# Kernel tuning notes

Measured on AMD Instinct MI355X. Metric: run time of the kernel, lower is better.

Reference implementation:

```python
import math
import jax, jax.numpy as jnp
import numpy as np

B, S, HIDDEN = 1, 8192, 2048
NUM_HEADS = 16
HEAD_DIM = HIDDEN // NUM_HEADS
NUM_FW = 4
FW_DIM = HIDDEN // NUM_FW
D_H = FW_DIM  # inter_multi = 1.0
WINDOW = 256
CHUNK = 2048
ROPE_THETA = 500000.0
BASE_LR_INV = float(np.log(np.expm1(0.001)))  # inv_softplus(1e-3)


def rms_norm(x, w, eps=1e-6):
    return x * jax.lax.rsqrt(jnp.mean(x * x, axis=-1, keepdims=True) + eps) * w


def apply_rope(q, k, theta):
    D = q.shape[-1]
    inv = 1.0 / (theta ** (jnp.arange(0, D, 2, dtype=jnp.float32) / D))
    t = jnp.arange(q.shape[1], dtype=jnp.float32)
    f = t[:, None] * inv[None, :]  # [S, D/2]
    cos = jnp.cos(f)[None, :, None, :]
    sin = jnp.sin(f)[None, :, None, :]
    def ap(x):
        x1, x2 = jnp.split(x, 2, axis=-1)
        return jnp.concatenate([x1 * cos - x2 * sin, x2 * cos + x1 * sin], axis=-1)
    return ap(q), ap(k)


def sliding_window_attn(q, k, v, window):
    # q,k,v: [B,S,H,D]; causal window of `window` tokens incl. self (flash (window-1, 0))
    B_, S_, H_, D_ = q.shape
    W = window
    nc = S_ // W
    def blk(x):
        return x.transpose(0, 2, 1, 3).reshape(B_, H_, nc, W, D_)
    qb, kb, vb = blk(q), blk(k), blk(v)
    pad = jnp.zeros((B_, H_, 1, W, D_), q.dtype)
    k2 = jnp.concatenate([jnp.concatenate([pad, kb[:, :, :-1]], 2), kb], 3)  # [B,H,nc,2W,D]
    v2 = jnp.concatenate([jnp.concatenate([pad, vb[:, :, :-1]], 2), vb], 3)
    r = jnp.arange(W)[:, None]
    j = jnp.arange(2 * W)[None, :]
    base = (j >= r + 1) & (j <= W + r)  # causal + within-window
    keypos = (jnp.arange(nc)[:, None, None] - 1) * W + j[None]
    mask = base[None] & (keypos >= 0)  # [nc,W,2W]
    scores = jnp.einsum('bhnqd,bhnkd->bhnqk', qb, k2) * (1.0 / math.sqrt(D_))
    scores = jnp.where(mask[None, None], scores, -jnp.inf)
    p = jax.nn.softmax(scores, axis=-1)
    o = jnp.einsum('bhnqk,bhnkd->bhnqd', p, v2)
    return o.reshape(B_, H_, S_, D_).transpose(0, 2, 1, 3)


def ttt_swiglu(fq, fk, fv, l0, l1, l2, w0, w1, w2, chunk):
    # fq/fk/fv: [BN,S,d]; l*: [BN,S,1]; w0,w2: [BN,dh,d]; w1: [BN,d,dh]
    BN, S_, d = fq.shape
    nc = S_ // chunk
    def ch(x):
        return x.reshape(BN, nc, chunk, x.shape[-1]).transpose(1, 0, 2, 3)
    xs = (ch(fq), ch(fk), ch(fv), ch(l0), ch(l1), ch(l2))
    def step(carry, x):
        w0c, w1c, w2c = carry
        qi, ki, vi, lr0, lr1, lr2 = x
        # apply current fast weights to chunk queries (SwiGLU MLP)
        o = jnp.einsum('bch,boh->bco',
                       jax.nn.silu(jnp.einsum('bcd,bhd->bch', qi, w0c)) * jnp.einsum('bcd,bhd->bch', qi, w2c),
                       w1c)
        # manual gradient of dot-product TTT loss L = -sum(v * f(k))
        g = jnp.einsum('bcd,bhd->bch', ki, w0c)
        hm = jnp.einsum('bcd,bhd->bch', ki, w2c)
        sg = jax.nn.sigmoid(g)
        silu_g = g * sg
        hid = silu_g * hm
        dhid = jnp.einsum('bco,boh->bch', vi, w1c)
        dhm = dhid * silu_g
        dg = dhid * hm
        dgp = dg * (sg * (1.0 + g * (1.0 - sg)))  # silu backprop
        w0n = w0c + jnp.einsum('bch,bcd->bhd', dgp * lr0, ki)
        w2n = w2c + jnp.einsum('bch,bcd->bhd', dhm * lr2, ki)
        w1n = w1c + jnp.einsum('bco,bch->boh', vi * lr1, hid)
        return (w0n, w1n, w2n), o
    _, outs = jax.lax.scan(step, (w0, w1, w2), xs)
    return outs.transpose(1, 0, 2, 3).reshape(BN, S_, d)


def setup_inputs():
    key = jax.random.key(0)
    ks = jax.random.split(key, 8)
    h = HIDDEN
    return {
        'hidden_states': jax.random.normal(ks[0], (B, S, h), jnp.float32),
        'qkv_w': jax.random.normal(ks[1], (3 * h, h), jnp.float32) * 0.02,
        'q_norm_w': jnp.ones((h,), jnp.float32),
        'k_norm_w': jnp.ones((h,), jnp.float32),
        'qk_scale': jnp.ones((h, 2), jnp.float32),
        'qk_offset': jnp.zeros((h, 2), jnp.float32),
        'lr_w': jax.random.normal(ks[2], (3 * NUM_FW, h), jnp.float32) * 0.02,
        'lr_b': jnp.zeros((3 * NUM_FW,), jnp.float32),
        'w0': jax.random.normal(ks[3], (NUM_FW, D_H, FW_DIM), jnp.float32) / math.sqrt(FW_DIM),
        'w1': jax.random.normal(ks[4], (NUM_FW, FW_DIM, D_H), jnp.float32) / math.sqrt(D_H),
        'w2': jax.random.normal(ks[5], (NUM_FW, D_H, FW_DIM), jnp.float32) / math.sqrt(FW_DIM),
        'ttt_norm_w': jnp.ones((FW_DIM,), jnp.float32),
        'o_proj_w': jax.random.normal(ks[6], (h, h), jnp.float32) * 0.02,
    }


def reference(hidden_states, qkv_w, q_norm_w, k_norm_w, qk_scale, qk_offset,
              lr_w, lr_b, w0, w1, w2, ttt_norm_w, o_proj_w):
    qkv = hidden_states @ qkv_w.T
    q, k, v = jnp.split(qkv, 3, axis=-1)
    q = rms_norm(q, q_norm_w)
    k = rms_norm(k, k_norm_w)
    # rescale q/k for the fast-weight path
    fq = q * qk_scale[:, 0] + qk_offset[:, 0]
    fk = k * qk_scale[:, 1] + qk_offset[:, 1]
    fv = v
    # windowed RoPE attention path
    qh = q.reshape(B, S, NUM_HEADS, HEAD_DIM)
    kh = k.reshape(B, S, NUM_HEADS, HEAD_DIM)
    vh = v.reshape(B, S, NUM_HEADS, HEAD_DIM)
    qh, kh = apply_rope(qh, kh, ROPE_THETA)
    attn_o = sliding_window_attn(qh, kh, vh, WINDOW).reshape(B, S, HIDDEN)
    # fast-weight (TTT) path: silu + per-head l2-norm on q/k
    fq = jax.nn.silu(fq).reshape(B, S, NUM_FW, FW_DIM)
    fk = jax.nn.silu(fk).reshape(B, S, NUM_FW, FW_DIM)
    fv = jax.nn.silu(fv).reshape(B, S, NUM_FW, FW_DIM)
    fq = fq / jnp.maximum(jnp.linalg.norm(fq, axis=-1, keepdims=True), 1e-12)
    fk = fk / jnp.maximum(jnp.linalg.norm(fk, axis=-1, keepdims=True), 1e-12)
    def flat(x):
        return x.transpose(0, 2, 1, 3).reshape(B * NUM_FW, S, FW_DIM)
    # per-token learning rates (mamba parameterization)
    lr = jax.nn.softplus(hidden_states @ lr_w.T + lr_b + BASE_LR_INV)  # [B,S,3*NH]
    l0, l1, l2 = jnp.split(lr, 3, axis=-1)
    def flat_lr(x):
        return x.transpose(0, 2, 1).reshape(B * NUM_FW, S, 1)
    def bcast(w):
        return jnp.broadcast_to(w[None], (B,) + w.shape).reshape(B * NUM_FW, w.shape[1], w.shape[2])
    o_fast = ttt_swiglu(flat(fq), flat(fk), flat(fv),
                        flat_lr(l0), flat_lr(l1), flat_lr(l2),
                        bcast(w0), bcast(w1), bcast(w2), CHUNK)
    o_fast = rms_norm(o_fast.reshape(B, NUM_FW, S, FW_DIM), ttt_norm_w)
    o_fast = o_fast.transpose(0, 2, 1, 3).reshape(B, S, HIDDEN)
    return (attn_o + o_fast) @ o_proj_w.T
```

## Files before the change

kernel.cpp:

```cpp
#include <hip/hip_runtime.h>
#include <hip/hip_bf16.h>

typedef __hip_bfloat16 bf16;
typedef __bf16 bft;
typedef bft bf16x8 __attribute__((ext_vector_type(8)));
typedef bft bf16x4 __attribute__((ext_vector_type(4)));
typedef float f32x4 __attribute__((ext_vector_type(4)));

#define S_LEN 8192
#define HID   2048
#define QKV3  6144
#define NH    16
#define HD    128
#define NFW   4
#define FD    512
#define CHUNK_LEN 2048
#define NCHUNK 4
#define BASE_LR_INV (-6.9072552f)
#define QKP 136
#define VSP 72
#define PSP 76

__device__ __forceinline__ float bf2f(bf16 x){ return __bfloat162float(x); }
__device__ __forceinline__ bf16  f2bf(float x){ return __float2bfloat16(x); }
__device__ __forceinline__ float sigm(float x){ return 1.f/(1.f+__expf(-x)); }
__device__ __forceinline__ float siluf(float x){ return x/(1.f+__expf(-x)); }
__device__ __forceinline__ float wave_sum(float v){
  #pragma unroll
  for(int off=32; off; off>>=1) v += __shfl_xor(v, off, 64);
  return v;
}

template<int N>
__device__ __forceinline__ void waitcnt_vm(){
  static_assert(N==0||N==2||N==4||N==8, "unsupported vmcnt");
  if constexpr (N==0)      asm volatile("s_waitcnt vmcnt(0)" ::: "memory");
  else if constexpr (N==2) asm volatile("s_waitcnt vmcnt(2)" ::: "memory");
  else if constexpr (N==4) asm volatile("s_waitcnt vmcnt(4)" ::: "memory");
  else                     asm volatile("s_waitcnt vmcnt(8)" ::: "memory");
}

__device__ __forceinline__ void bar(){
  __builtin_amdgcn_s_barrier();
  asm volatile("" ::: "memory");
}

template<int ROWS>
__device__ __forceinline__ void stage(const bft* __restrict__ src, long ld,
                                      bft* dst, int tid)
{
  const int lane = tid & 63, wv = tid >> 6;
  #pragma unroll
  for (int i = 0; i < ROWS/64; ++i) {
    const int r0 = wv*16 + i*64;
    const int row = r0 + (lane >> 2);
    const int g = (lane & 3) ^ ((row >> 1) & 3);
    const bft* gp = src + (size_t)row*ld + g*8;
    bft* lp = dst + (size_t)r0*32;
    __builtin_amdgcn_global_load_lds(
        (const __attribute__((address_space(1))) void*)gp,
        (__attribute__((address_space(3))) void*)lp, 16, 0, 0);
  }
}

template<int BM,int BN,int EPI>
__global__ __launch_bounds__(256) void mgemm_k(
    const bft* __restrict__ A, const bft* __restrict__ B, void* __restrict__ Cv,
    bft* __restrict__ Cd, bft* __restrict__ Ct, int K,
    long lda, long ldb, long ldc, long sA, long sB, long sC, long sCd)
{
  constexpr int AM = BM/32, AN = BN/32;
  constexpr int LPT = BM/64 + BN/64;
  __shared__ __align__(16) bft As[4][BM*32];
  __shared__ __align__(16) bft Bs[4][BN*32];
  const int tid = threadIdx.x;
  const int z = blockIdx.z;
  A += (size_t)z * sA;
  B += (size_t)z * sB;
  const size_t m0 = (size_t)blockIdx.y * BM, n0 = (size_t)blockIdx.x * BN;
  const int wv = tid >> 6, lane = tid & 63;
  const int wm = (wv & 1) * (BM/2), wn = (wv >> 1) * (BN/2);
  const int fr = lane & 15;
  const int fsw = ((lane >> 4) ^ ((fr >> 1) & 3)) * 8;

  f32x4 acc[AM][AN];
  #pragma unroll
  for (int i=0;i<AM;i++)
    #pragma unroll
    for (int j=0;j<AN;j++) acc[i][j] = (f32x4){0.f,0.f,0.f,0.f};

  const bft* Ab = A + m0*lda;
  const bft* Bb = B + n0*ldb;
  const int NS = K >> 5;

  stage<BM>(Ab,      lda, As[0], tid);
  stage<BN>(Bb,      ldb, Bs[0], tid);
  stage<BM>(Ab + 32, lda, As[1], tid);
  stage<BN>(Bb + 32, ldb, Bs[1], tid);
  waitcnt_vm<LPT>();
  bar();

  bf16x8 aP[AM], bP[AN], aQ[AM], bQ[AN];
  #pragma unroll
  for (int mi=0; mi<AM; mi++)
    aP[mi] = *(const bf16x8*)(As[0] + (size_t)(wm + mi*16 + fr)*32 + fsw);
  #pragma unroll
  for (int ni=0; ni<AN; ni++)
    bP[ni] = *(const bf16x8*)(Bs[0] + (size_t)(wn + ni*16 + fr)*32 + fsw);

  auto body = [&](bf16x8 (&ac)[AM], bf16x8 (&bc)[AN],
                  bf16x8 (&an)[AM], bf16x8 (&bn)[AN], int s){
    const int kt = (s + 2) * 32;
    const bool st2 = (s + 2 < NS);
    const bool rd  = (s + 1 < NS);
    if (st2) {
      stage<BM>(Ab + kt, lda, As[(s+2)&3], tid);
      stage<BN>(Bb + kt, ldb, Bs[(s+2)&3], tid);
    }
    if (rd) {
      if (st2) waitcnt_vm<LPT>(); else waitcnt_vm<0>();
      bar();
      const bft* An = As[(s+1)&3];
      const bft* Bn = Bs[(s+1)&3];
      #pragma unroll
      for (int mi=0; mi<AM; mi++)
        an[mi] = *(const bf16x8*)(An + (size_t)(wm + mi*16 + fr)*32 + fsw);
      #pragma unroll
      for (int ni=0; ni<AN; ni++)
        bn[ni] = *(const bf16x8*)(Bn + (size_t)(wn + ni*16 + fr)*32 + fsw);
    }
    __builtin_amdgcn_s_setprio(1);
    #pragma unroll
    for (int mi=0; mi<AM; mi++)
      #pragma unroll
      for (int ni=0; ni<AN; ni++)
        acc[mi][ni] = __builtin_amdgcn_mfma_f32_16x16x32_bf16(ac[mi], bc[ni], acc[mi][ni], 0, 0, 0);
    __builtin_amdgcn_s_setprio(0);
  };

  for (int s = 0; s < NS; s += 2) {
    body(aP, bP, aQ, bQ, s);
    body(aQ, bQ, aP, bP, s + 1);
  }

  const int er = (lane >> 4) * 4;
  const int ec = lane & 15;
  #pragma unroll
  for (int mi=0; mi<AM; mi++){
    #pragma unroll
    for (int ni=0; ni<AN; ni++){
      #pragma unroll
      for (int r=0; r<4; r++){
        size_t row = m0 + wm + mi*16 + er + r;
        size_t col = n0 + wn + ni*16 + ec;
        size_t idx = (size_t)z*sC + row*ldc + col;
        float v = acc[mi][ni][r];
        if constexpr (EPI == 0){
          ((bft*)Cv)[idx] = (bft)v;
        } else if constexpr (EPI == 1){
          ((float*)Cv)[idx] = v;
        } else {
          float nv = ((float*)Cv)[idx] + v;
          ((float*)Cv)[idx] = nv;
          Cd[(size_t)z*sCd + row*ldc + col] = (bft)nv;
          if (Ct) Ct[(size_t)z*FD*FD + col*FD + row] = (bft)nv;
        }
      }
    }
  }
}

template<int BM,int BN,int EPI>
static inline void mgemm(hipStream_t st, const bft* A, const bft* B, void* C,
    bft* Cd, bft* Ct, int M, int N, int K, long lda, long ldb, long ldc,
    int batch, long sA, long sB, long sC, long sCd)
{
  dim3 g(N/BN, M/BM, batch);
  mgemm_k<BM,BN,EPI><<<g, 256, 0, st>>>(A, B, C, Cd, Ct, K, lda, ldb, ldc, sA, sB, sC, sCd);
}

__device__ __forceinline__ void stage8(const bft* __restrict__ src, long ld,
                                       bft* dst, int tid)
{
  const int lane = tid & 63, wv = tid >> 6;
  #pragma unroll
  for (int i = 0; i < 2; ++i) {
    const int r0 = wv*16 + i*128;
    const int row = r0 + (lane >> 2);
    const int g = (lane & 3) ^ ((row >> 1) & 3);
    const bft* gp = src + (size_t)row*ld + g*8;
    bft* lp = dst + (size_t)r0*32;
    __builtin_amdgcn_global_load_lds(
        (const __attribute__((address_space(1))) void*)gp,
        (__attribute__((address_space(3))) void*)lp, 16, 0, 0);
  }
}

template<int EPI>
__global__ __launch_bounds__(512, 2) void mgemm8_k(
    const bft* __restrict__ A, const bft* __restrict__ B, void* __restrict__ Cv,
    int K, long lda, long ldb, long ldc)
{
  __shared__ __align__(16) bft As[4][256*32];
  __shared__ __align__(16) bft Bs[4][256*32];
  const int tid = threadIdx.x;

  const int gx = (int)gridDim.x;
  const int nwg = (int)(gridDim.x * gridDim.y);
  int lin = (int)(blockIdx.y * gridDim.x + blockIdx.x);
  if ((nwg & 7) == 0) lin = (lin & 7) * (nwg >> 3) + (lin >> 3);
  const size_t m0 = (size_t)(lin / gx) * 256;
  const size_t n0 = (size_t)(lin % gx) * 256;

  const int wv = tid >> 6, lane = tid & 63;
  const int wm = (wv & 1) * 128, wn = (wv >> 1) * 64;
  const int fr = lane & 15;
  const int fsw = ((lane >> 4) ^ ((fr >> 1) & 3)) * 8;

  f32x4 acc[8][4];
  #pragma unroll
  for (int i=0;i<8;i++)
    #pragma unroll
    for (int j=0;j<4;j++) acc[i][j] = (f32x4){0.f,0.f,0.f,0.f};

  const bft* Ab = A + m0*lda;
  const bft* Bb = B + n0*ldb;
  const int NS = K >> 5;

  stage8(Ab,      lda, As[0], tid);
  stage8(Bb,      ldb, Bs[0], tid);
  stage8(Ab + 32, lda, As[1], tid);
  stage8(Bb + 32, ldb, Bs[1], tid);
  waitcnt_vm<4>();
  bar();

  bf16x8 aP[8], bP[4], aQ[8], bQ[4];
  #pragma unroll
  for (int mi=0; mi<8; mi++)
    aP[mi] = *(const bf16x8*)(As[0] + (size_t)(wm + mi*16 + fr)*32 + fsw);
  #pragma unroll
  for (int ni=0; ni<4; ni++)
    bP[ni] = *(const bf16x8*)(Bs[0] + (size_t)(wn + ni*16 + fr)*32 + fsw);

  auto body = [&](bf16x8 (&ac)[8], bf16x8 (&bc)[4],
                  bf16x8 (&an)[8], bf16x8 (&bn)[4], int s){
    const int kt = (s + 2) * 32;
    const bool st2 = (s + 2 < NS);
    const bool rd  = (s + 1 < NS);
    if (st2) {
      stage8(Ab + kt, lda, As[(s+2)&3], tid);
      stage8(Bb + kt, ldb, Bs[(s+2)&3], tid);
    }
    if (rd) {
      if (st2) waitcnt_vm<4>(); else waitcnt_vm<0>();
      bar();
      const bft* An = As[(s+1)&3];
      const bft* Bn = Bs[(s+1)&3];
      #pragma unroll
      for (int mi=0; mi<8; mi++)
        an[mi] = *(const bf16x8*)(An + (size_t)(wm + mi*16 + fr)*32 + fsw);
      #pragma unroll
      for (int ni=0; ni<4; ni++)
        bn[ni] = *(const bf16x8*)(Bn + (size_t)(wn + ni*16 + fr)*32 + fsw);
    }
    __builtin_amdgcn_s_setprio(1);
    #pragma unroll
    for (int mi=0; mi<8; mi++)
      #pragma unroll
      for (int ni=0; ni<4; ni++)
        acc[mi][ni] = __builtin_amdgcn_mfma_f32_16x16x32_bf16(ac[mi], bc[ni], acc[mi][ni], 0, 0, 0);
    __builtin_amdgcn_s_setprio(0);
  };

  for (int s = 0; s < NS; s += 2) {
    body(aP, bP, aQ, bQ, s);
    body(aQ, bQ, aP, bP, s + 1);
  }

  const int er = (lane >> 4) * 4;
  const int ec = lane & 15;
  #pragma unroll
  for (int mi=0; mi<8; mi++){
    #pragma unroll
    for (int ni=0; ni<4; ni++){
      #pragma unroll
      for (int r=0; r<4; r++){
        size_t row = m0 + wm + mi*16 + er + r;
        size_t col = n0 + wn + ni*16 + ec;
        size_t idx = row*ldc + col;
        float v = acc[mi][ni][r];
        if constexpr (EPI == 0) ((bft*)Cv)[idx] = (bft)v;
        else                    ((float*)Cv)[idx] = v;
      }
    }
  }
}

template<int EPI>
static inline void mgemm8(hipStream_t st, const bft* A, const bft* B, void* C,
                          int M, int N, int K, long lda, long ldb, long ldc)
{
  dim3 g(N/256, M/256, 1);
  mgemm8_k<EPI><<<g, 512, 0, st>>>(A, B, C, K, lda, ldb, ldc);
}

__global__ __launch_bounds__(256) void cvt_k(const float* __restrict__ s,
    bft* __restrict__ d)
{
  size_t i = ((size_t)blockIdx.x*256 + threadIdx.x) * 8;
  const float4 v0 = *(const float4*)(s + i);
  const float4 v1 = *(const float4*)(s + i + 4);
  bf16x8 b;
  b[0]=(bft)v0.x; b[1]=(bft)v0.y; b[2]=(bft)v0.z; b[3]=(bft)v0.w;
  b[4]=(bft)v1.x; b[5]=(bft)v1.y; b[6]=(bft)v1.z; b[7]=(bft)v1.w;
  *(bf16x8*)(d + i) = b;
}

__global__ __launch_bounds__(256) void tr_k(const bft* __restrict__ in,
    bft* __restrict__ out, long ldin, long sIn, long sOut)
{
  __shared__ __align__(16) bft t[64][72];
  const int c0 = blockIdx.x*64, r0 = blockIdx.y*64;
  in  += (size_t)blockIdx.z * sIn;
  out += (size_t)blockIdx.z * sOut;
  const int tid = threadIdx.x;
  #pragma unroll
  for (int i=0;i<2;i++){
    int e = tid + i*256;
    int r = e >> 3, c8 = (e & 7) * 8;
    *(bf16x8*)&t[r][c8] = *(const bf16x8*)(in + (size_t)(r0+r)*ldin + c0 + c8);
  }
  __syncthreads();
  #pragma unroll
  for (int i=0;i<2;i++){
    int e = tid + i*256;
    int c = e >> 3, r8 = (e & 7) * 8;
    bf16x8 v;
    #pragma unroll
    for (int j=0;j<8;j++) v[j] = t[r8+j][c];
    *(bf16x8*)(out + (size_t)(c0+c)*CHUNK_LEN + r0 + r8) = v;
  }
}

__global__ __launch_bounds__(256) void tcw1_k(const float* __restrict__ w1,
    bft* __restrict__ w1tb)
{
  size_t idx = (size_t)blockIdx.x*256 + threadIdx.x;
  int z = (int)(idx >> 18);
  int h = (int)((idx >> 9) & 511);
  int o = (int)(idx & 511);
  w1tb[idx] = (bft)w1[(size_t)z*FD*FD + (size_t)o*FD + h];
}

__global__ __launch_bounds__(256) void vt_k(const bf16* __restrict__ qkv,
    bft* __restrict__ vT)
{
  __shared__ __align__(16) bft t[64*QKP];
  const int s0 = blockIdx.x * 64;
  const int h  = blockIdx.y;
  const int tid = threadIdx.x;
  #pragma unroll
  for (int i=0;i<4;i++){
    int e = tid + i*256;
    int rr = e >> 4, doff = (e & 15) * 8;
    *(bf16x8*)(t + rr*QKP + doff) =
        *(const bf16x8*)((const bft*)qkv + (size_t)(s0+rr)*QKV3 + 2*HID + h*HD + doff);
  }
  __syncthreads();
  #pragma unroll
  for (int it=0; it<4; it++){
    int d = (tid >> 3) + it*32;
    int so8 = (tid & 7) * 8;
    bf16x8 v;
    #pragma unroll
    for (int j=0;j<8;j++) v[j] = t[(so8+j)*QKP + d];
    *(bf16x8*)(vT + ((size_t)(h*HD + d))*S_LEN + s0 + so8) = v;
  }
}

__global__ void rope_k(float* __restrict__ rc, float* __restrict__ rs){
  int pos = blockIdx.x, d = threadIdx.x;
  float inv = 1.f / powf(500000.0f, (float)d * (1.0f/64.0f));
  float ang = (float)pos * inv;
  rc[pos*64+d] = cosf(ang);
  rs[pos*64+d] = sinf(ang);
}

__global__ __launch_bounds__(256) void lr_k(const float* __restrict__ hidden,
    const float* __restrict__ lr_w, const float* __restrict__ lr_b,
    float* __restrict__ lro)
{
  __shared__ float hrow[HID];
  __shared__ float red[4][12];
  int s = blockIdx.x, tid = threadIdx.x;
  for(int i=0;i<HID/256;i++) hrow[tid+256*i] = hidden[(size_t)s*HID + tid + 256*i];
  __syncthreads();
  float part[12];
  #pragma unroll
  for(int o=0;o<12;o++) part[o]=0.f;
  for(int i=0;i<HID/256;i++){
    int j = tid + 256*i;
    float h = hrow[j];
    #pragma unroll
    for(int o=0;o<12;o++) part[o] += h * lr_w[o*HID + j];
  }
  int lane = tid & 63, w = tid >> 6;
  #pragma unroll
  for(int o=0;o<12;o++){
    float v = wave_sum(part[o]);
    if(lane==0) red[w][o] = v;
  }
  __syncthreads();
  if(tid < 12){
    float v = red[0][tid]+red[1][tid]+red[2][tid]+red[3][tid] + lr_b[tid] + BASE_LR_INV;
    float sp = (v > 20.f) ? v : log1pf(expf(v));
    lro[s*12 + tid] = sp;
  }
}

__global__ __launch_bounds__(256) void e2a_k(
    bf16* __restrict__ qkv,
    const float* __restrict__ qnw, const float* __restrict__ knw)
{
  __shared__ float red[8];
  int s = blockIdx.x, tid = threadIdx.x;
  int lane = tid & 63, w = tid >> 6;
  float qv[8], kv[8];
  float sq = 0.f, sk = 0.f;
  size_t base = (size_t)s*QKV3;
  #pragma unroll
  for(int i=0;i<8;i++){
    int j = tid*8 + i;
    qv[i] = bf2f(qkv[base + j]);
    kv[i] = bf2f(qkv[base + HID + j]);
    sq += qv[i]*qv[i]; sk += kv[i]*kv[i];
  }
  sq = wave_sum(sq); sk = wave_sum(sk);
  if(lane==0){ red[w] = sq; red[4+w] = sk; }
  __syncthreads();
  float rq = rsqrtf((red[0]+red[1]+red[2]+red[3])*(1.f/HID) + 1e-6f);
  float rk = rsqrtf((red[4]+red[5]+red[6]+red[7])*(1.f/HID) + 1e-6f);
  #pragma unroll
  for(int i=0;i<8;i++){
    int j = tid*8 + i;
    qkv[base + j]       = f2bf(qv[i]*rq*qnw[j]);
    qkv[base + HID + j] = f2bf(kv[i]*rk*knw[j]);
  }
}

__global__ __launch_bounds__(256) void e2b_k(
    bf16* __restrict__ qkv,
    const float* __restrict__ qks, const float* __restrict__ qko)
{
  int s = blockIdx.x, tid = threadIdx.x;
  size_t base = (size_t)s*QKV3;
  float a[8], b[8], vv[8];
  float ga = 0.f, gb2 = 0.f;
  #pragma unroll
  for(int i=0;i<8;i++){
    int j = tid*8 + i;
    float qn = bf2f(qkv[base + j]);
    float kn = bf2f(qkv[base + HID + j]);
    float v  = bf2f(qkv[base + 2*HID + j]);
    a[i] = siluf(qn*qks[2*j]   + qko[2*j]);
    b[i] = siluf(kn*qks[2*j+1] + qko[2*j+1]);
    vv[i] = siluf(v);
    ga += a[i]*a[i]; gb2 += b[i]*b[i];
  }
  ga = wave_sum(ga); gb2 = wave_sum(gb2);
  float iq = 1.f / fmaxf(sqrtf(ga), 1e-12f);
  float ik = 1.f / fmaxf(sqrtf(gb2), 1e-12f);
  #pragma unroll
  for(int i=0;i<8;i++){
    int j = tid*8 + i;
    qkv[base + j]         = f2bf(a[i]*iq);
    qkv[base + HID + j]   = f2bf(b[i]*ik);
    qkv[base + 2*HID + j] = f2bf(vv[i]);
  }
}

__global__ __launch_bounds__(256) void attn_k(
    const bf16* __restrict__ qkv, const bft* __restrict__ vT,
    const float* __restrict__ rc, const float* __restrict__ rs,
    float* __restrict__ attn)
{
  __shared__ __align__(16) bft Qs[64*QKP];
  __shared__ __align__(16) bft Ks[64*QKP];
  __shared__ __align__(16) bft Vs[128*VSP];
  __shared__ __align__(16) bft Ps[64*PSP];
  const int head = blockIdx.x >> 7;
  const int Q0 = (blockIdx.x & 127) * 64;
  const int tid = threadIdx.x;
  const int hb = head * HD;
  const int lane = tid & 63;
  const int wm = (tid >> 6) * 16;
  const int fr = lane & 15, fko = (lane >> 4) * 8;
  const int rbase = (lane >> 4) * 4;

  #pragma unroll
  for(int i=0;i<16;i++){
    int e = tid + i*256;
    int rr = e >> 6, d = e & 63;
    int qpos = Q0 + rr;
    size_t b = (size_t)qpos*QKV3 + hb;
    float x1 = bf2f(qkv[b + d]);
    float x2 = bf2f(qkv[b + d + 64]);
    float c = rc[qpos*64 + d], sn = rs[qpos*64 + d];
    Qs[rr*QKP + d]      = (bft)(x1*c - x2*sn);
    Qs[rr*QKP + d + 64] = (bft)(x2*c + x1*sn);
  }
  __syncthreads();
  bf16x8 qf[4];
  #pragma unroll
  for (int kk=0;kk<4;kk++)
    qf[kk] = *(const bf16x8*)(Qs + (wm+fr)*QKP + kk*32 + fko);

  f32x4 Ot[8];
  #pragma unroll
  for (int i=0;i<8;i++) Ot[i] = (f32x4){0.f,0.f,0.f,0.f};
  float m4[4], l4[4];
  #pragma unroll
  for (int r=0;r<4;r++){ m4[r] = -INFINITY; l4[r] = 0.f; }

  for (int kt=0; kt<5; kt++){
    const int kb = Q0 - 256 + kt*64;
    if (kb < 0) continue;
    __syncthreads();
    #pragma unroll
    for(int i=0;i<16;i++){
      int e = tid + i*256;
      int rr = e >> 6, d = e & 63;
      int kpos = kb + rr;
      size_t b = (size_t)kpos*QKV3 + HID + hb;
      float x1 = bf2f(qkv[b + d]);
      float x2 = bf2f(qkv[b + d + 64]);
      float c = rc[kpos*64 + d], sn = rs[kpos*64 + d];
      Ks[rr*QKP + d]      = (bft)(x1*c - x2*sn);
      Ks[rr*QKP + d + 64] = (bft)(x2*c + x1*sn);
    }
    {
      int d = tid >> 1, koff = (tid & 1) * 32;
      const bft* vrow = vT + ((size_t)(hb + d))*S_LEN + kb + koff;
      bft* lrow = Vs + d*VSP + koff;
      #pragma unroll
      for (int j8=0;j8<4;j8++)
        *(bf16x8*)(lrow + j8*8) = *(const bf16x8*)(vrow + j8*8);
    }
    __syncthreads();

    f32x4 st[4];
    #pragma unroll
    for (int nt=0;nt<4;nt++){
      f32x4 acc = (f32x4){0.f,0.f,0.f,0.f};
      #pragma unroll
      for (int kk=0;kk<4;kk++){
        bf16x8 kf = *(const bf16x8*)(Ks + (nt*16+fr)*QKP + kk*32 + fko);
        acc = __builtin_amdgcn_mfma_f32_16x16x32_bf16(qf[kk], kf, acc, 0, 0, 0);
      }
      st[nt] = acc;
    }

    float pv[4][4];
    #pragma unroll
    for (int r=0;r<4;r++){
      int qpos = Q0 + wm + rbase + r;
      float sm[4];
      float mx = -INFINITY;
      #pragma unroll
      for (int nt=0;nt<4;nt++){
        int kpos = kb + nt*16 + fr;
        bool valid = (kpos > qpos - 256) && (kpos <= qpos);
        float s = valid ? st[nt][r] * 0.088388347648318447f : -INFINITY;
        sm[nt] = s;
        mx = fmaxf(mx, s);
      }
      mx = fmaxf(mx, __shfl_xor(mx, 1, 64));
      mx = fmaxf(mx, __shfl_xor(mx, 2, 64));
      mx = fmaxf(mx, __shfl_xor(mx, 4, 64));
      mx = fmaxf(mx, __shfl_xor(mx, 8, 64));
      float mnew = fmaxf(m4[r], mx);
      float alpha = (mnew == -INFINITY) ? 1.f : __expf(m4[r] - mnew);
      float ps = 0.f;
      #pragma unroll
      for (int nt=0;nt<4;nt++){
        float p = (sm[nt] == -INFINITY) ? 0.f : __expf(sm[nt] - mnew);
        pv[nt][r] = p;
        ps += p;
      }
      ps += __shfl_xor(ps, 1, 64);
      ps += __shfl_xor(ps, 2, 64);
      ps += __shfl_xor(ps, 4, 64);
      ps += __shfl_xor(ps, 8, 64);
      l4[r] = l4[r]*alpha + ps;
      m4[r] = mnew;
      #pragma unroll
      for (int ct=0;ct<8;ct++) Ot[ct][r] *= alpha;
    }

    #pragma unroll
    for (int r=0;r<4;r++){
      int row = wm + rbase + r;
      #pragma unroll
      for (int nt=0;nt<4;nt++)
        Ps[row*PSP + nt*16 + fr] = (bft)pv[nt][r];
    }
    bf16x8 af[2];
    #pragma unroll
    for (int kk=0;kk<2;kk++){
      const bft* pp = Ps + (wm+fr)*PSP + kk*32 + fko;
      bf16x4 lo = *(const bf16x4*)pp;
      bf16x4 hi = *(const bf16x4*)(pp+4);
      bf16x8 a;
      #pragma unroll
      for (int j=0;j<4;j++){ a[j]=lo[j]; a[j+4]=hi[j]; }
      af[kk]=a;
    }
    #pragma unroll
    for (int ct=0;ct<8;ct++)
      #pragma unroll
      for (int kk=0;kk<2;kk++){
        bf16x8 bv = *(const bf16x8*)(Vs + (ct*16+fr)*VSP + kk*32 + fko);
        Ot[ct] = __builtin_amdgcn_mfma_f32_16x16x32_bf16(af[kk], bv, Ot[ct], 0, 0, 0);
      }
  }

  #pragma unroll
  for (int r=0;r<4;r++){
    float invl = 1.f / l4[r];
    int qpos = Q0 + wm + rbase + r;
    size_t ob = (size_t)qpos*HID + hb;
    #pragma unroll
    for (int ct=0;ct<8;ct++)
      attn[ob + ct*16 + fr] = Ot[ct][r] * invl;
  }
}

__global__ __launch_bounds__(256) void e3f_k(
    bft* __restrict__ gh, bft* __restrict__ qgm, bft* __restrict__ hid)
{
  size_t idx = (size_t)blockIdx.x*256 + threadIdx.x;
  int z  = (int)(idx >> 20);
  int ci = (int)((idx >> 9) & 2047);
  int d  = (int)(idx & 511);
  size_t b = ((size_t)z*CHUNK_LEN + ci)*1024 + d;
  float opre = siluf((float)qgm[b]) * (float)qgm[b + 512];
  hid[idx] = (bft)(siluf((float)gh[b]) * (float)gh[b + 512]);
  qgm[b]   = (bft)opre;
}

__global__ __launch_bounds__(256) void e4f_k(
    bft* __restrict__ gh, bft* __restrict__ qgm,
    const bf16* __restrict__ qkv, const float* __restrict__ lrb, int cbase)
{
  size_t idx = (size_t)blockIdx.x*256 + threadIdx.x;
  int z  = (int)(idx >> 20);
  int ci = (int)((idx >> 9) & 2047);
  int d  = (int)(idx & 511);
  int s  = cbase + ci;
  float l0  = lrb[s*12 + z];
  float l1  = lrb[s*12 + 4 + z];
  float l2v = lrb[s*12 + 8 + z];
  size_t b = ((size_t)z*CHUNK_LEN + ci)*1024 + d;
  float gg = (float)gh[b], hv = (float)gh[b + 512], dh = (float)qgm[b + 512];
  float sg = sigm(gg);
  float silu_g = gg * sg;
  float dhm = dh * silu_g;
  float dg  = dh * hv;
  float dgp = dg * (sg * (1.f + gg * (1.f - sg)));
  float fvv = bf2f(qkv[(size_t)s*QKV3 + 2*HID + z*FD + d]);
  gh[b]        = (bft)(dgp * l0);
  gh[b + 512]  = (bft)(dhm * l2v);
  qgm[b + 512] = (bft)(fvv * l1);
}

__global__ __launch_bounds__(256) void e5_k(const float* __restrict__ attn,
    const bf16* __restrict__ ofc, const float* __restrict__ tnw,
    bf16* __restrict__ qkv, int cbase)
{
  int ci = blockIdx.x, tid = threadIdx.x;
  int s = cbase + ci;
  int lane = tid & 63, w = tid >> 6;
  float o[8]; float ss = 0.f;
  size_t ob = ((size_t)w*CHUNK_LEN + ci)*FD + (size_t)lane*8;
  #pragma unroll
  for(int i=0;i<8;i++){ o[i] = bf2f(ofc[ob+i]); ss += o[i]*o[i]; }
  ss = wave_sum(ss);
  float inv = rsqrtf(ss*(1.f/FD) + 1e-6f);
  size_t xb = (size_t)s*QKV3 + w*FD + (size_t)lane*8;
  size_t ab = (size_t)s*HID  + w*FD + (size_t)lane*8;
  #pragma unroll
  for(int i=0;i<8;i++){
    int d = lane*8 + i;
    qkv[xb+i] = f2bf(attn[ab+i] + o[i]*inv*tnw[d]);
  }
}

extern "C" void kernel_launch(void* const* d_in, const int* in_sizes, int n_in,
                              void* d_out, int out_size, void* d_ws, size_t ws_size,
                              hipStream_t stream)
{
  (void)in_sizes; (void)n_in; (void)out_size;
  const float* hidden   = (const float*)d_in[0];
  const float* qkv_w    = (const float*)d_in[1];
  const float* q_norm_w = (const float*)d_in[2];
  const float* k_norm_w = (const float*)d_in[3];
  const float* qk_scale = (const float*)d_in[4];
  const float* qk_off   = (const float*)d_in[5];
  const float* lr_w     = (const float*)d_in[6];
  const float* lr_b     = (const float*)d_in[7];
  const float* w0_in    = (const float*)d_in[8];
  const float* w1_in    = (const float*)d_in[9];
  const float* w2_in    = (const float*)d_in[10];
  const float* ttt_nw   = (const float*)d_in[11];
  const float* o_proj   = (const float*)d_in[12];
  float* out = (float*)d_out;

  char* p = (char*)d_ws;
  auto alloc = [&](size_t n){ char* r = p; p += (n + 255) & ~(size_t)255; return (void*)r; };

  bf16*  qkv   = (bf16*) alloc((size_t)S_LEN*QKV3*sizeof(bf16));
  float* lrb   = (float*)alloc((size_t)S_LEN*12*sizeof(float));
  float* rc    = (float*)alloc((size_t)S_LEN*64*sizeof(float));
  float* rs    = (float*)alloc((size_t)S_LEN*64*sizeof(float));
  float* w0s   = (float*)alloc((size_t)NFW*FD*FD*sizeof(float));
  float* w1s   = (float*)alloc((size_t)NFW*FD*FD*sizeof(float));
  float* w2s   = (float*)alloc((size_t)NFW*FD*FD*sizeof(float));
  bft*   w1tb  = (bft*)  alloc((size_t)NFW*FD*FD*sizeof(bft));
  bft*   w02b  = (bft*)  alloc((size_t)NFW*1024*FD*sizeof(bft));
  bft*   w1b   = (bft*)  alloc((size_t)NFW*FD*FD*sizeof(bft));
  bf16*  gb    = (bf16*) alloc((size_t)NFW*CHUNK_LEN*FD*sizeof(bf16));
  bf16*  hmb   = (bf16*) alloc((size_t)NFW*CHUNK_LEN*FD*sizeof(bf16));
  bf16*  qgb   = (bf16*) alloc((size_t)NFW*CHUNK_LEN*FD*sizeof(bf16));
  bf16*  qmb   = (bf16*) alloc((size_t)NFW*CHUNK_LEN*FD*sizeof(bf16));
  bf16*  hidb  = (bf16*) alloc((size_t)NFW*CHUNK_LEN*FD*sizeof(bf16));
  bf16*  ofc   = (bf16*) alloc((size_t)NFW*CHUNK_LEN*FD*sizeof(bf16));
  bft*   fkT   = (bft*)  alloc((size_t)NFW*FD*CHUNK_LEN*sizeof(bft));
  bft*   hidT  = (bft*)  alloc((size_t)NFW*FD*CHUNK_LEN*sizeof(bft));
  bft*   a2T   = (bft*)  alloc((size_t)NFW*FD*CHUNK_LEN*sizeof(bft));

  if ((size_t)(p - (char*)d_ws) > ws_size) return;

  bft* ghb = (bft*)gb;
  bft* qgm = (bft*)qgb;
  bft* hidden_bf = (bft*)gb;
  bft* qkvw_bf   = (bft*)fkT;
  bft* vT        = (bft*)fkT;
  bft* opw_bf    = (bft*)hidb;

  float* attn = out;

  const long sW  = (long)FD*FD;
  const long sW2 = (long)1024*FD;
  const long sCh = (long)CHUNK_LEN*FD;
  const long sGH = (long)CHUNK_LEN*1024;
  const long sT  = (long)FD*CHUNK_LEN;

  hipMemcpyAsync(w0s, w0_in, (size_t)NFW*FD*FD*sizeof(float), hipMemcpyDeviceToDevice, stream);
  hipMemcpyAsync(w1s, w1_in, (size_t)NFW*FD*FD*sizeof(float), hipMemcpyDeviceToDevice, stream);
  hipMemcpyAsync(w2s, w2_in, (size_t)NFW*FD*FD*sizeof(float), hipMemcpyDeviceToDevice, stream);

  rope_k<<<S_LEN, 64, 0, stream>>>(rc, rs);
  lr_k<<<S_LEN, 256, 0, stream>>>(hidden, lr_w, lr_b, lrb);
  tcw1_k<<<NFW*FD*FD/256, 256, 0, stream>>>(w1_in, w1tb);
  cvt_k<<<(NFW*FD*FD)/2048, 256, 0, stream>>>(w1_in, w1b);
  for (int z = 0; z < NFW; ++z) {
    cvt_k<<<(FD*FD)/2048, 256, 0, stream>>>(w0_in + (size_t)z*sW, w02b + (size_t)z*sW2);
    cvt_k<<<(FD*FD)/2048, 256, 0, stream>>>(w2_in + (size_t)z*sW, w02b + (size_t)z*sW2 + (size_t)512*FD);
  }
  cvt_k<<<(S_LEN*HID)/2048, 256, 0, stream>>>(hidden, hidden_bf);
  cvt_k<<<(QKV3*HID)/2048, 256, 0, stream>>>(qkv_w, qkvw_bf);

  mgemm8<0>(stream, hidden_bf, qkvw_bf, (void*)qkv, S_LEN, QKV3, HID, HID, HID, QKV3);

  e2a_k<<<S_LEN, 256, 0, stream>>>(qkv, q_norm_w, k_norm_w);
  vt_k<<<dim3(S_LEN/64, NH), 256, 0, stream>>>(qkv, vT);
  attn_k<<<NH*128, 256, 0, stream>>>(qkv, vT, rc, rs, attn);
  e2b_k<<<S_LEN, 256, 0, stream>>>(qkv, qk_scale, qk_off);

  const int  NEL = NFW*CHUNK_LEN*FD/256;
  const dim3 tg(FD/64, CHUNK_LEN/64, NFW);

  for(int c=0; c<NCHUNK; c++){
    const bft* fqc = (const bft*)qkv + (size_t)c*CHUNK_LEN*QKV3;
    const bft* fkc = fqc + HID;
    const bft* fvc = fqc + 2*HID;
    mgemm<128,128,0>(stream, fkc, w02b, ghb, nullptr, nullptr,
        CHUNK_LEN, 1024, FD, QKV3, FD, 1024, NFW, FD, sW2, sGH, 0);
    mgemm<128,128,0>(stream, fqc, w02b, qgm, nullptr, nullptr,
        CHUNK_LEN, 1024, FD, QKV3, FD, 1024, NFW, FD, sW2, sGH, 0);
    e3f_k<<<NEL, 256, 0, stream>>>(ghb, qgm, (bft*)hidb);
    mgemm<128,128,0>(stream, (const bft*)qgm, w1b, ofc, nullptr, nullptr,
        CHUNK_LEN, FD, FD, 1024, FD, FD, NFW, sGH, sW, sCh, 0);
    mgemm<128,128,0>(stream, fvc, (const bft*)w1tb, qgm + 512, nullptr, nullptr,
        CHUNK_LEN, FD, FD, QKV3, FD, 1024, NFW, FD, sW, sGH, 0);
    e4f_k<<<NEL, 256, 0, stream>>>(ghb, qgm, qkv, lrb, c*CHUNK_LEN);
    tr_k<<<tg, 256, 0, stream>>>(fkc,              fkT,  QKV3, FD,  sT);
    tr_k<<<tg, 256, 0, stream>>>((const bft*)hidb, hidT, FD,   sCh, sT);
    tr_k<<<tg, 256, 0, stream>>>(ghb,       a2T, 1024, sGH, sT);
    mgemm<64,64,2>(stream, a2T, fkT,  w0s, w02b, nullptr,
        FD, FD, CHUNK_LEN, CHUNK_LEN, CHUNK_LEN, FD, NFW, sT, sT, sW, sW2);
    tr_k<<<tg, 256, 0, stream>>>(ghb + 512, a2T, 1024, sGH, sT);
    mgemm<64,64,2>(stream, a2T, fkT,  w2s, w02b + (size_t)512*FD, nullptr,
        FD, FD, CHUNK_LEN, CHUNK_LEN, CHUNK_LEN, FD, NFW, sT, sT, sW, sW2);
    tr_k<<<tg, 256, 0, stream>>>(qgm + 512, a2T, 1024, sGH, sT);
    mgemm<64,64,2>(stream, a2T, hidT, w1s, w1b, w1tb,
        FD, FD, CHUNK_LEN, CHUNK_LEN, CHUNK_LEN, FD, NFW, sT, sT, sW, sW);
    e5_k<<<CHUNK_LEN, 256, 0, stream>>>(attn, ofc, ttt_nw, qkv, c*CHUNK_LEN);
  }

  cvt_k<<<(HID*HID)/2048, 256, 0, stream>>>(o_proj, opw_bf);
  mgemm8<1>(stream, (const bft*)qkv, opw_bf, out, S_LEN, HID, HID, QKV3, HID, HID);
}
```

Measured before the change: 1.506 ms.

## Restructure GEMM mainloop into split-phase LDS reads with interleaved staging

Replaces the register double-buffered fragment prefetch in the templated GEMM with a single-buffer loop. When the tile has four or more M fragments, each K-step is split into two phases, each loading half of the A fragments, issuing one operand's global-to-LDS stage and running half the MFMAs between barriers. The aim is to cut register pressure and spread the async copies across the compute. The cost is extra barriers per K-step and LDS reads that are no longer prefetched ahead of the MFMAs. A sched_barrier is also added before the MFMA block of the 8x4 GEMM kernel to stop the compiler from reordering loads into it.

```diff
diff --git a/kernel.cpp b/kernel.cpp
--- a/kernel.cpp
+++ b/kernel.cpp
@@ -71,6 +71,8 @@
 {
   constexpr int AM = BM/32, AN = BN/32;
   constexpr int LPT = BM/64 + BN/64;
+  constexpr int NPH = (AM >= 4) ? 2 : 1;
+  constexpr int MH  = AM / NPH;
   __shared__ __align__(16) bft As[4][BM*32];
   __shared__ __align__(16) bft Bs[4][BN*32];
   const int tid = threadIdx.x;
@@ -100,47 +102,50 @@
   waitcnt_vm<LPT>();
   bar();
 
-  bf16x8 aP[AM], bP[AN], aQ[AM], bQ[AN];
-  #pragma unroll
-  for (int mi=0; mi<AM; mi++)
-    aP[mi] = *(const bf16x8*)(As[0] + (size_t)(wm + mi*16 + fr)*32 + fsw);
-  #pragma unroll
-  for (int ni=0; ni<AN; ni++)
-    bP[ni] = *(const bf16x8*)(Bs[0] + (size_t)(wn + ni*16 + fr)*32 + fsw);
-
-  auto body = [&](bf16x8 (&ac)[AM], bf16x8 (&bc)[AN],
-                  bf16x8 (&an)[AM], bf16x8 (&bn)[AN], int s){
+  for (int s = 0; s < NS; ++s) {
+    const bft* Ap = As[s & 3];
+    const bft* Bp = Bs[s & 3];
     const int kt = (s + 2) * 32;
-    const bool st2 = (s + 2 < NS);
-    const bool rd  = (s + 1 < NS);
-    if (st2) {
-      stage<BM>(Ab + kt, lda, As[(s+2)&3], tid);
-      stage<BN>(Bb + kt, ldb, Bs[(s+2)&3], tid);
-    }
-    if (rd) {
-      if (st2) waitcnt_vm<LPT>(); else waitcnt_vm<0>();
+    const bool st = (s + 2 < NS);
+
+    bf16x8 bvv[AN], afv[MH];
+    #pragma unroll
+    for (int ni=0; ni<AN; ni++)
+      bvv[ni] = *(const bf16x8*)(Bp + (size_t)(wn + ni*16 + fr)*32 + fsw);
+    #pragma unroll
+    for (int i=0; i<MH; i++)
+      afv[i] = *(const bf16x8*)(Ap + (size_t)(wm + i*16 + fr)*32 + fsw);
+    if (st) stage<BM>(Ab + kt, lda, As[(s+2)&3], tid);
+    if constexpr (NPH == 1) {
+      if (st) { stage<BN>(Bb + kt, ldb, Bs[(s+2)&3], tid); waitcnt_vm<LPT>(); }
+      else waitcnt_vm<0>();
+    }
+    bar();
+    __builtin_amdgcn_s_setprio(1);
+    #pragma unroll
+    for (int i=0; i<MH; i++)
+      #pragma unroll
+      for (int ni=0; ni<AN; ni++)
+        acc[i][ni] = __builtin_amdgcn_mfma_f32_16x16x32_bf16(afv[i], bvv[ni], acc[i][ni], 0, 0, 0);
+    __builtin_amdgcn_s_setprio(0);
+
+    if constexpr (NPH == 2) {
       bar();
-      const bft* An = As[(s+1)&3];
-      const bft* Bn = Bs[(s+1)&3];
-      #pragma unroll
-      for (int mi=0; mi<AM; mi++)
-        an[mi] = *(const bf16x8*)(An + (size_t)(wm + mi*16 + fr)*32 + fsw);
-      #pragma unroll
-      for (int ni=0; ni<AN; ni++)
-        bn[ni] = *(const bf16x8*)(Bn + (size_t)(wn + ni*16 + fr)*32 + fsw);
-    }
-    __builtin_amdgcn_s_setprio(1);
-    #pragma unroll
-    for (int mi=0; mi<AM; mi++)
-      #pragma unroll
-      for (int ni=0; ni<AN; ni++)
-        acc[mi][ni] = __builtin_amdgcn_mfma_f32_16x16x32_bf16(ac[mi], bc[ni], acc[mi][ni], 0, 0, 0);
-    __builtin_amdgcn_s_setprio(0);
-  };
-
-  for (int s = 0; s < NS; s += 2) {
-    body(aP, bP, aQ, bQ, s);
-    body(aQ, bQ, aP, bP, s + 1);
+      #pragma unroll
+      for (int i=0; i<MH; i++)
+        afv[i] = *(const bf16x8*)(Ap + (size_t)(wm + (MH+i)*16 + fr)*32 + fsw);
+      if (st) { stage<BN>(Bb + kt, ldb, Bs[(s+2)&3], tid); waitcnt_vm<LPT>(); }
+      else waitcnt_vm<0>();
+      bar();
+      __builtin_amdgcn_s_setprio(1);
+      #pragma unroll
+      for (int i=0; i<MH; i++)
+        #pragma unroll
+        for (int ni=0; ni<AN; ni++)
+          acc[MH+i][ni] = __builtin_amdgcn_mfma_f32_16x16x32_bf16(afv[i], bvv[ni], acc[MH+i][ni], 0, 0, 0);
+      __builtin_amdgcn_s_setprio(0);
+      bar();
+    }
   }
 
   const int er = (lane >> 4) * 4;
@@ -263,6 +268,7 @@
       for (int ni=0; ni<4; ni++)
         bn[ni] = *(const bf16x8*)(Bn + (size_t)(wn + ni*16 + fr)*32 + fsw);
     }
+    __builtin_amdgcn_sched_barrier(0);
     __builtin_amdgcn_s_setprio(1);
     #pragma unroll
     for (int mi=0; mi<8; mi++)
```

Measured after the change: 1.499 ms. Within noise of the previous version (-0.5%).
